# Performance work log

Hardware: AMD Instinct MI355X
Metric: run time of the kernel (lower is better)

## Reference

```python
import jax, jax.numpy as jnp
import numpy as np

INPUT_SIZE, HIDDEN, OUTPUT = 6, 64, 3
B, T = 4096, 512


def setup_inputs() -> dict:
    key = jax.random.key(0)
    ks = jax.random.split(key, 12)
    s = 1.0 / np.sqrt(HIDDEN)  # torch LSTM/Linear default init scale
    u = lambda k, shape: jax.random.uniform(k, shape, jnp.float32, -s, s)
    return {
        "x": jax.random.normal(ks[0], (B, T, INPUT_SIZE), jnp.float32),
        "Wih0": u(ks[1], (4 * HIDDEN, INPUT_SIZE)),
        "Whh0": u(ks[2], (4 * HIDDEN, HIDDEN)),
        "bih0": u(ks[3], (4 * HIDDEN,)),
        "bhh0": u(ks[4], (4 * HIDDEN,)),
        "Wih1": u(ks[5], (4 * HIDDEN, HIDDEN)),
        "Whh1": u(ks[6], (4 * HIDDEN, HIDDEN)),
        "bih1": u(ks[7], (4 * HIDDEN,)),
        "bhh1": u(ks[8], (4 * HIDDEN,)),
        "Wfc": u(ks[9], (OUTPUT, HIDDEN)),
        "bfc": u(ks[10], (OUTPUT,)),
    }


def _lstm_layer(x, Wih, Whh, bih, bhh):
    # x: [B, T, F] -> hidden sequence [B, T, H]; torch gate order i,f,g,o
    Bn = x.shape[0]
    H = Whh.shape[1]
    b = bih + bhh
    # precompute input projections for all steps: [T, B, 4H]
    gx = jnp.einsum('btf,gf->tbg', x, Wih) + b

    def step(carry, gxt):
        h, c = carry
        gates = gxt + h @ Whh.T
        i, f, g, o = jnp.split(gates, 4, axis=-1)
        i, f, o = jax.nn.sigmoid(i), jax.nn.sigmoid(f), jax.nn.sigmoid(o)
        g = jnp.tanh(g)
        c = f * c + i * g
        h = o * jnp.tanh(c)
        return (h, c), h

    h0 = jnp.zeros((Bn, H), x.dtype)
    c0 = jnp.zeros((Bn, H), x.dtype)
    (_, _), hs = jax.lax.scan(step, (h0, c0), gx)  # hs: [T, B, H]
    return hs.transpose(1, 0, 2)


def reference(x, Wih0, Whh0, bih0, bhh0, Wih1, Whh1, bih1, bhh1, Wfc, bfc):
    h1 = _lstm_layer(x, Wih0, Whh0, bih0, bhh0)
    h2 = _lstm_layer(h1, Wih1, Whh1, bih1, bhh1)
    last = h2[:, -1, :]              # [B, H]
    return last @ Wfc.T + bfc        # [B, OUTPUT]
```

## Files before the change

### kernel.cpp

```cpp
#include <hip/hip_runtime.h>

#define H    64
#define TT   512
#define NB   16
#define OUTD 3
#define BTOT 4096
#define INF  6
#define HS   72
#define XS   32

typedef _Float16 f16;
typedef _Float16 f16x8 __attribute__((ext_vector_type(8)));
typedef float    f32x4 __attribute__((ext_vector_type(4)));
typedef float    f32x2 __attribute__((ext_vector_type(2)));

#define LOG2E 1.44269504088896340736f
#define KSC   (2.0f * LOG2E)

static __device__ __forceinline__ f32x2 pk_fma(f32x2 a, f32x2 b, f32x2 c) {
#if __has_builtin(__builtin_elementwise_fma)
    return __builtin_elementwise_fma(a, b, c);
#else
    f32x2 r; r.x = __builtin_fmaf(a.x, b.x, c.x); r.y = __builtin_fmaf(a.y, b.y, c.y);
    return r;
#endif
}

static __device__ __forceinline__ f32x2 pk_min(f32x2 a, f32x2 b) {
#if __has_builtin(__builtin_elementwise_min)
    return __builtin_elementwise_min(a, b);
#else
    f32x2 r; r.x = fminf(a.x, b.x); r.y = fminf(a.y, b.y);
    return r;
#endif
}

__device__ __forceinline__ f32x2 lstm_cell2(f32x2 ai, f32x2 af, f32x2 ag, f32x2 ao,
                                            f32x2& C) {
    f32x2 ei, ef, eg, eo;
    ei.x = __builtin_amdgcn_exp2f(ai.x); ei.y = __builtin_amdgcn_exp2f(ai.y);
    ef.x = __builtin_amdgcn_exp2f(af.x); ef.y = __builtin_amdgcn_exp2f(af.y);
    eg.x = __builtin_amdgcn_exp2f(ag.x); eg.y = __builtin_amdgcn_exp2f(ag.y);
    eo.x = __builtin_amdgcn_exp2f(ao.x); eo.y = __builtin_amdgcn_exp2f(ao.y);
    f32x2 A  = ei + 1.0f;
    f32x2 F  = ef + 1.0f;
    f32x2 Bp = eg + 1.0f;
    f32x2 G  = eg - 1.0f;
    f32x2 P  = A * Bp;
    f32x2 PF = P * F;
    f32x2 r1; r1.x = __builtin_amdgcn_rcpf(PF.x); r1.y = __builtin_amdgcn_rcpf(PF.y);
    f32x2 n1 = ef * C * P;
    f32x2 t2 = ei * G * F;
    f32x2 k2 = {KSC, KSC};
    C = pk_fma(k2, t2, n1) * r1;
    f32x2 clim = {126.0f, 126.0f};
    f32x2 Cc = pk_min(C, clim);
    f32x2 ec; ec.x = __builtin_amdgcn_exp2f(Cc.x); ec.y = __builtin_amdgcn_exp2f(Cc.y);
    f32x2 D2 = (eo + 1.0f) * (ec + 1.0f);
    f32x2 r2; r2.x = __builtin_amdgcn_rcpf(D2.x); r2.y = __builtin_amdgcn_rcpf(D2.y);
    return eo * (ec - 1.0f) * r2;
}

__launch_bounds__(256, 1)
__global__ void lstm_fused(const float* __restrict__ x,
                           const float* __restrict__ Wih0, const float* __restrict__ Whh0,
                           const float* __restrict__ bih0, const float* __restrict__ bhh0,
                           const float* __restrict__ Wih1, const float* __restrict__ Whh1,
                           const float* __restrict__ bih1, const float* __restrict__ bhh1,
                           const float* __restrict__ Wfc,  const float* __restrict__ bfc,
                           float* __restrict__ out)
{
    __shared__ __align__(16) f16 H0[2][NB * HS];
    __shared__ __align__(16) f16 H1[2][NB * HS];
    __shared__ __align__(16) f16 Xr[2][NB * XS];
    __shared__ float hfin[NB][H + 1];

    const int t   = threadIdx.x;
    const int wv  = t >> 6;
    const int l15 = t & 15;
    const int q   = (t >> 4) & 3;
    const int jj  = 16 * wv + l15;
    const int b0  = blockIdx.x * NB;
    const int ar  = l15 * HS;
    const int ko  = q * 8;

    for (int idx = t; idx < 2 * NB * HS; idx += 256) {
        (&H0[0][0])[idx] = (f16)0.0f;
        (&H1[0][0])[idx] = (f16)0.0f;
    }
    for (int idx = t; idx < 2 * NB * XS; idx += 256) (&Xr[0][0])[idx] = (f16)0.0f;
    __syncthreads();

    const bool loader = t < NB * INF;
    const int  xb = t / INF;
    const int  xf = t - xb * INF;
    if (loader)
        Xr[0][xb * XS + xf] = (f16)x[((size_t)(b0 + xb) * TT) * INF + xf];

    f16x8 wh0[2][4], wx0[4], wi1[2][4], wh1[2][4];
    f32x4 bC0[4], bC1[4];
    #pragma unroll
    for (int g = 0; g < 4; ++g) {
        const float sc = (g == 2) ? KSC : LOG2E;
        const int n = 64 * g + jj;
        #pragma unroll
        for (int kt = 0; kt < 2; ++kt) {
            f16x8 v0, v1, v2;
            #pragma unroll
            for (int j = 0; j < 8; ++j) {
                const int k = kt * 32 + q * 8 + j;
                v0[j] = (f16)(Whh0[n * H + k] * sc);
                v1[j] = (f16)(Wih1[n * H + k] * sc);
                v2[j] = (f16)(Whh1[n * H + k] * sc);
            }
            wh0[kt][g] = v0; wi1[kt][g] = v1; wh1[kt][g] = v2;
        }
        f16x8 vx;
        #pragma unroll
        for (int j = 0; j < 8; ++j)
            vx[j] = (q == 0 && j < INF) ? (f16)(Wih0[n * INF + j] * sc) : (f16)0.0f;
        wx0[g] = vx;
        const float bu0 = (bih0[64 * g + jj] + bhh0[64 * g + jj]) * sc;
        const float bu1 = (bih1[64 * g + jj] + bhh1[64 * g + jj]) * sc;
        bC0[g] = (f32x4){bu0, bu0, bu0, bu0};
        bC1[g] = (f32x4){bu1, bu1, bu1, bu1};
    }
    f32x2 c0a = {0.f, 0.f}, c0b = {0.f, 0.f};
    f32x2 c1a = {0.f, 0.f}, c1b = {0.f, 0.f};
    float xpre = 0.0f;
    __syncthreads();

    auto mfmaA = [&](f16x8 a0, f16x8 a1, f16x8 ax, f32x4* acc) {
        #pragma unroll
        for (int g = 0; g < 4; ++g) {
            f32x4 a = __builtin_amdgcn_mfma_f32_16x16x32_f16(a0, wh0[0][g], bC0[g], 0, 0, 0);
            a = __builtin_amdgcn_mfma_f32_16x16x32_f16(a1, wh0[1][g], a, 0, 0, 0);
            a = __builtin_amdgcn_mfma_f32_16x16x32_f16(ax, wx0[g],    a, 0, 0, 0);
            acc[g] = a;
        }
    };
    auto mfmaB = [&](f16x8 a0, f16x8 a1, f16x8 r0, f16x8 r1, f32x4* acc) {
        #pragma unroll
        for (int g = 0; g < 4; ++g) {
            f32x4 a = __builtin_amdgcn_mfma_f32_16x16x32_f16(a0, wi1[0][g], bC1[g], 0, 0, 0);
            a = __builtin_amdgcn_mfma_f32_16x16x32_f16(a1, wi1[1][g], a, 0, 0, 0);
            a = __builtin_amdgcn_mfma_f32_16x16x32_f16(r0, wh1[0][g], a, 0, 0, 0);
            a = __builtin_amdgcn_mfma_f32_16x16x32_f16(r1, wh1[1][g], a, 0, 0, 0);
            acc[g] = a;
        }
    };
    auto cellWrite = [&](f32x4* acc, f32x2& ca, f32x2& cb, f16* dst) {
        f32x2 h01 = lstm_cell2((f32x2){acc[0][0], acc[0][1]},
                               (f32x2){acc[1][0], acc[1][1]},
                               (f32x2){acc[2][0], acc[2][1]},
                               (f32x2){acc[3][0], acc[3][1]}, ca);
        f32x2 h23 = lstm_cell2((f32x2){acc[0][2], acc[0][3]},
                               (f32x2){acc[1][2], acc[1][3]},
                               (f32x2){acc[2][2], acc[2][3]}, 
                               (f32x2){acc[3][2], acc[3][3]}, cb);
        dst[(q * 4 + 0) * HS + jj] = (f16)h01.x;
        dst[(q * 4 + 1) * HS + jj] = (f16)h01.y;
        dst[(q * 4 + 2) * HS + jj] = (f16)h23.x;
        dst[(q * 4 + 3) * HS + jj] = (f16)h23.y;
    };

    {
        if (loader) xpre = x[((size_t)(b0 + xb) * TT + 1) * INF + xf];
        const f16* h0r = &H0[1][0];
        f16x8 a0 = *(const f16x8*)&h0r[ar + ko];
        f16x8 a1 = *(const f16x8*)&h0r[ar + 32 + ko];
        f16x8 ax = *(const f16x8*)&Xr[0][l15 * XS + ko];
        f32x4 accA[4];
        mfmaA(a0, a1, ax, accA);
        cellWrite(accA, c0a, c0b, &H0[0][0]);
        if (loader) Xr[1][xb * XS + xf] = (f16)xpre;
        __syncthreads();
    }

    #pragma unroll 2
    for (int s = 1; s < TT; ++s) {
        const int p = s & 1, pp = p ^ 1;
        if (loader) {
            const int tn = (s + 1 < TT) ? (s + 1) : (TT - 1);
            xpre = x[((size_t)(b0 + xb) * TT + tn) * INF + xf];
        }
        const f16* h0r = &H0[pp][0];
        const f16* h1r = &H1[p][0];
        f16x8 a0 = *(const f16x8*)&h0r[ar + ko];
        f16x8 a1 = *(const f16x8*)&h0r[ar + 32 + ko];
        f16x8 ax = *(const f16x8*)&Xr[p][l15 * XS + ko];
        f16x8 r0 = *(const f16x8*)&h1r[ar + ko];
        f16x8 r1 = *(const f16x8*)&h1r[ar + 32 + ko];
        f32x4 accA[4], accB[4];
        mfmaA(a0, a1, ax, accA);
        mfmaB(a0, a1, r0, r1, accB);
        cellWrite(accA, c0a, c0b, &H0[p][0]);
        cellWrite(accB, c1a, c1b, &H1[pp][0]);
        if (loader) Xr[pp][xb * XS + xf] = (f16)xpre;
        __syncthreads();
    }

    {
        const f16* h0r = &H0[1][0];
        const f16* h1r = &H1[0][0];
        f16x8 a0 = *(const f16x8*)&h0r[ar + ko];
        f16x8 a1 = *(const f16x8*)&h0r[ar + 32 + ko];
        f16x8 r0 = *(const f16x8*)&h1r[ar + ko];
        f16x8 r1 = *(const f16x8*)&h1r[ar + 32 + ko];
        f32x4 accB[4];
        mfmaB(a0, a1, r0, r1, accB);
        f32x2 h01 = lstm_cell2((f32x2){accB[0][0], accB[0][1]},
                               (f32x2){accB[1][0], accB[1][1]},
                               (f32x2){accB[2][0], accB[2][1]},
                               (f32x2){accB[3][0], accB[3][1]}, c1a);
        f32x2 h23 = lstm_cell2((f32x2){accB[0][2], accB[0][3]},
                               (f32x2){accB[1][2], accB[1][3]},
                               (f32x2){accB[2][2], accB[2][3]},
                               (f32x2){accB[3][2], accB[3][3]}, c1b);
        hfin[q * 4 + 0][jj] = h01.x;
        hfin[q * 4 + 1][jj] = h01.y;
        hfin[q * 4 + 2][jj] = h23.x;
        hfin[q * 4 + 3][jj] = h23.y;
        __syncthreads();
    }

    if (t < NB * OUTD) {
        const int b = t / OUTD;
        const int o = t - b * OUTD;
        float a = bfc[o];
        #pragma unroll
        for (int j = 0; j < H; ++j)
            a += Wfc[o * H + j] * hfin[b][j];
        out[(size_t)(b0 + b) * OUTD + o] = a;
    }
}

extern "C" void kernel_launch(void* const* d_in, const int* in_sizes, int n_in,
                              void* d_out, int out_size, void* d_ws, size_t ws_size,
                              hipStream_t stream) {
    const float* x    = (const float*)d_in[0];
    const float* Wih0 = (const float*)d_in[1];
    const float* Whh0 = (const float*)d_in[2];
    const float* bih0 = (const float*)d_in[3];
    const float* bhh0 = (const float*)d_in[4];
    const float* Wih1 = (const float*)d_in[5];
    const float* Whh1 = (const float*)d_in[6];
    const float* bih1 = (const float*)d_in[7];
    const float* bhh1 = (const float*)d_in[8];
    const float* Wfc  = (const float*)d_in[9];
    const float* bfc  = (const float*)d_in[10];

    dim3 grid(BTOT / NB);
    dim3 block(256);
    lstm_fused<<<grid, block, 0, stream>>>(x, Wih0, Whh0, bih0, bhh0,
                                           Wih1, Whh1, bih1, bhh1,
                                           Wfc, bfc, (float*)d_out);
}
```

Baseline: 469.6 us.

## Halve batch per block and redistribute cell math across lanes via shuffles

Each block now handles 8 sequences instead of 16 while still issuing 16-row MFMAs, with the extra rows zero-padded. Cross-half-wave shuffles pack the useful accumulator rows, so every lane computes one f32x2 cell update instead of two. Launch bounds now allow two blocks per CU and the grid doubles. The goal is to shorten the per-step serial cell math and raise occupancy on the latency-bound recurrence. The cost is half-wasted MFMA throughput and added shuffle latency on every step.

Measured after the change: 636.8 us. 35.6% more time.

```diff
diff --git a/kernel.cpp b/kernel.cpp
--- a/kernel.cpp
+++ b/kernel.cpp
@@ -2,7 +2,7 @@
 
 #define H    64
 #define TT   512
-#define NB   16
+#define NB   8
 #define OUTD 3
 #define BTOT 4096
 #define INF  6
@@ -61,34 +61,45 @@
     return eo * (ec - 1.0f) * r2;
 }
 
-__launch_bounds__(256, 1)
-__global__ void lstm_fused(const float* __restrict__ x,
-                           const float* __restrict__ Wih0, const float* __restrict__ Whh0,
-                           const float* __restrict__ bih0, const float* __restrict__ bhh0,
-                           const float* __restrict__ Wih1, const float* __restrict__ Whh1,
-                           const float* __restrict__ bih1, const float* __restrict__ bhh1,
-                           const float* __restrict__ Wfc,  const float* __restrict__ bfc,
-                           float* __restrict__ out)
+static __device__ __forceinline__ f32x2 pack2(f32x4 a, int lane) {
+    float u2 = __shfl_xor(a[2], 32, 64);
+    float u3 = __shfl_xor(a[3], 32, 64);
+    f32x2 r;
+    r.x = (lane < 32) ? a[0] : u2;
+    r.y = (lane < 32) ? a[1] : u3;
+    return r;
+}
+
+__launch_bounds__(256, 2)
+__global__ void lstm_fused2(const float* __restrict__ x,
+                            const float* __restrict__ Wih0, const float* __restrict__ Whh0,
+                            const float* __restrict__ bih0, const float* __restrict__ bhh0,
+                            const float* __restrict__ Wih1, const float* __restrict__ Whh1,
+                            const float* __restrict__ bih1, const float* __restrict__ bhh1,
+                            const float* __restrict__ Wfc,  const float* __restrict__ bfc,
+                            float* __restrict__ out)
 {
-    __shared__ __align__(16) f16 H0[2][NB * HS];
-    __shared__ __align__(16) f16 H1[2][NB * HS];
-    __shared__ __align__(16) f16 Xr[2][NB * XS];
+    __shared__ __align__(16) f16 H0[2][16 * HS];
+    __shared__ __align__(16) f16 H1[2][16 * HS];
+    __shared__ __align__(16) f16 Xr[2][16 * XS];
     __shared__ float hfin[NB][H + 1];
 
-    const int t   = threadIdx.x;
-    const int wv  = t >> 6;
-    const int l15 = t & 15;
-    const int q   = (t >> 4) & 3;
-    const int jj  = 16 * wv + l15;
-    const int b0  = blockIdx.x * NB;
-    const int ar  = l15 * HS;
-    const int ko  = q * 8;
-
-    for (int idx = t; idx < 2 * NB * HS; idx += 256) {
+    const int t    = threadIdx.x;
+    const int lane = t & 63;
+    const int wv   = t >> 6;
+    const int l15  = lane & 15;
+    const int q    = (lane >> 4) & 3;
+    const int jj   = 16 * wv + l15;
+    const int b0   = blockIdx.x * NB;
+    const int ar   = l15 * HS;
+    const int ko   = q * 8;
+    const int r0   = 4 * ((lane >> 4) & 1) + 2 * (lane >> 5);
+
+    for (int idx = t; idx < 2 * 16 * HS; idx += 256) {
         (&H0[0][0])[idx] = (f16)0.0f;
         (&H1[0][0])[idx] = (f16)0.0f;
     }
-    for (int idx = t; idx < 2 * NB * XS; idx += 256) (&Xr[0][0])[idx] = (f16)0.0f;
+    for (int idx = t; idx < 2 * 16 * XS; idx += 256) (&Xr[0][0])[idx] = (f16)0.0f;
     __syncthreads();
 
     const bool loader = t < NB * INF;
@@ -125,8 +136,8 @@
         bC0[g] = (f32x4){bu0, bu0, bu0, bu0};
         bC1[g] = (f32x4){bu1, bu1, bu1, bu1};
     }
-    f32x2 c0a = {0.f, 0.f}, c0b = {0.f, 0.f};
-    f32x2 c1a = {0.f, 0.f}, c1b = {0.f, 0.f};
+    f32x2 c0 = {0.f, 0.f};
+    f32x2 c1 = {0.f, 0.f};
     float xpre = 0.0f;
     __syncthreads();
 
@@ -139,29 +150,25 @@
             acc[g] = a;
         }
     };
-    auto mfmaB = [&](f16x8 a0, f16x8 a1, f16x8 r0, f16x8 r1, f32x4* acc) {
+    auto mfmaB = [&](f16x8 a0, f16x8 a1, f16x8 r0v, f16x8 r1v, f32x4* acc) {
         #pragma unroll
         for (int g = 0; g < 4; ++g) {
-            f32x4 a = __builtin_amdgcn_mfma_f32_16x16x32_f16(a0, wi1[0][g], bC1[g], 0, 0, 0);
-            a = __builtin_amdgcn_mfma_f32_16x16x32_f16(a1, wi1[1][g], a, 0, 0, 0);
-            a = __builtin_amdgcn_mfma_f32_16x16x32_f16(r0, wh1[0][g], a, 0, 0, 0);
-            a = __builtin_amdgcn_mfma_f32_16x16x32_f16(r1, wh1[1][g], a, 0, 0, 0);
+            f32x4 a = __builtin_amdgcn_mfma_f32_16x16x32_f16(a0,  wi1[0][g], bC1[g], 0, 0, 0);
+            a = __builtin_amdgcn_mfma_f32_16x16x32_f16(a1,  wi1[1][g], a, 0, 0, 0);
+            a = __builtin_amdgcn_mfma_f32_16x16x32_f16(r0v, wh1[0][g], a, 0, 0, 0);
+            a = __builtin_amdgcn_mfma_f32_16x16x32_f16(r1v, wh1[1][g], a, 0, 0, 0);
             acc[g] = a;
         }
     };
-    auto cellWrite = [&](f32x4* acc, f32x2& ca, f32x2& cb, f16* dst) {
-        f32x2 h01 = lstm_cell2((f32x2){acc[0][0], acc[0][1]},
-                               (f32x2){acc[1][0], acc[1][1]},
-                               (f32x2){acc[2][0], acc[2][1]},
-                               (f32x2){acc[3][0], acc[3][1]}, ca);
-        f32x2 h23 = lstm_cell2((f32x2){acc[0][2], acc[0][3]},
-                               (f32x2){acc[1][2], acc[1][3]},
-                               (f32x2){acc[2][2], acc[2][3]}, 
-                               (f32x2){acc[3][2], acc[3][3]}, cb);
-        dst[(q * 4 + 0) * HS + jj] = (f16)h01.x;
-        dst[(q * 4 + 1) * HS + jj] = (f16)h01.y;
-        dst[(q * 4 + 2) * HS + jj] = (f16)h23.x;
-        dst[(q * 4 + 3) * HS + jj] = (f16)h23.y;
+    auto cellWrite = [&](f32x4* acc, f32x2& cs, f16* dst) -> f32x2 {
+        f32x2 g0 = pack2(acc[0], lane);
+        f32x2 g1 = pack2(acc[1], lane);
+        f32x2 g2 = pack2(acc[2], lane);
+        f32x2 g3 = pack2(acc[3], lane);
+        f32x2 hv = lstm_cell2(g0, g1, g2, g3, cs);
+        dst[(r0 + 0) * HS + jj] = (f16)hv.x;
+        dst[(r0 + 1) * HS + jj] = (f16)hv.y;
+        return hv;
     };
 
     {
@@ -172,7 +179,7 @@
         f16x8 ax = *(const f16x8*)&Xr[0][l15 * XS + ko];
         f32x4 accA[4];
         mfmaA(a0, a1, ax, accA);
-        cellWrite(accA, c0a, c0b, &H0[0][0]);
+        cellWrite(accA, c0, &H0[0][0]);
         if (loader) Xr[1][xb * XS + xf] = (f16)xpre;
         __syncthreads();
     }
@@ -189,13 +196,13 @@
         f16x8 a0 = *(const f16x8*)&h0r[ar + ko];
         f16x8 a1 = *(const f16x8*)&h0r[ar + 32 + ko];
         f16x8 ax = *(const f16x8*)&Xr[p][l15 * XS + ko];
-        f16x8 r0 = *(const f16x8*)&h1r[ar + ko];
-        f16x8 r1 = *(const f16x8*)&h1r[ar + 32 + ko];
+        f16x8 r0v = *(const f16x8*)&h1r[ar + ko];
+        f16x8 r1v = *(const f16x8*)&h1r[ar + 32 + ko];
         f32x4 accA[4], accB[4];
         mfmaA(a0, a1, ax, accA);
-        mfmaB(a0, a1, r0, r1, accB);
-        cellWrite(accA, c0a, c0b, &H0[p][0]);
-        cellWrite(accB, c1a, c1b, &H1[pp][0]);
+        mfmaB(a0, a1, r0v, r1v, accB);
+        cellWrite(accA, c0, &H0[p][0]);
+        cellWrite(accB, c1, &H1[pp][0]);
         if (loader) Xr[pp][xb * XS + xf] = (f16)xpre;
         __syncthreads();
     }
@@ -205,22 +212,17 @@
         const f16* h1r = &H1[0][0];
         f16x8 a0 = *(const f16x8*)&h0r[ar + ko];
         f16x8 a1 = *(const f16x8*)&h0r[ar + 32 + ko];
-        f16x8 r0 = *(const f16x8*)&h1r[ar + ko];
-        f16x8 r1 = *(const f16x8*)&h1r[ar + 32 + ko];
+        f16x8 r0v = *(const f16x8*)&h1r[ar + ko];
+        f16x8 r1v = *(const f16x8*)&h1r[ar + 32 + ko];
         f32x4 accB[4];
-        mfmaB(a0, a1, r0, r1, accB);
-        f32x2 h01 = lstm_cell2((f32x2){accB[0][0], accB[0][1]},
-                               (f32x2){accB[1][0], accB[1][1]},
-                               (f32x2){accB[2][0], accB[2][1]},
-                               (f32x2){accB[3][0], accB[3][1]}, c1a);
-        f32x2 h23 = lstm_cell2((f32x2){accB[0][2], accB[0][3]},
-                               (f32x2){accB[1][2], accB[1][3]},
-                               (f32x2){accB[2][2], accB[2][3]},
-                               (f32x2){accB[3][2], accB[3][3]}, c1b);
-        hfin[q * 4 + 0][jj] = h01.x;
-        hfin[q * 4 + 1][jj] = h01.y;
-        hfin[q * 4 + 2][jj] = h23.x;
-        hfin[q * 4 + 3][jj] = h23.y;
+        mfmaB(a0, a1, r0v, r1v, accB);
+        f32x2 g0 = pack2(accB[0], lane);
+        f32x2 g1 = pack2(accB[1], lane);
+        f32x2 g2 = pack2(accB[2], lane);
+        f32x2 g3 = pack2(accB[3], lane);
+        f32x2 hv = lstm_cell2(g0, g1, g2, g3, c1);
+        hfin[r0 + 0][jj] = hv.x;
+        hfin[r0 + 1][jj] = hv.y;
         __syncthreads();
     }
 
@@ -252,7 +254,7 @@
 
     dim3 grid(BTOT / NB);
     dim3 block(256);
-    lstm_fused<<<grid, block, 0, stream>>>(x, Wih0, Whh0, bih0, bhh0,
-                                           Wih1, Whh1, bih1, bhh1,
-                                           Wfc, bfc, (float*)d_out);
-}
+    lstm_fused2<<<grid, block, 0, stream>>>(x, Wih0, Whh0, bih0, bhh0,
+                                            Wih1, Whh1, bih1, bhh1,
+                                            Wfc, bfc, (float*)d_out);
+}
```
